# Performance work log

Measured on AMD Instinct MI355X. Metric: run time of the kernel, lower is better.

## Reference

```python
import jax, jax.numpy as jnp
import numpy as np

D_IN = 1024
D_OUT = 1024
NUM_HEAD = 16
HEAD_DIM = D_OUT // NUM_HEAD
CTX = 2048


def setup_inputs() -> dict:
    key = jax.random.key(0)
    ks = jax.random.split(key, 7)
    s = 0.02
    x = jax.random.normal(ks[0], (2, CTX, D_IN), dtype=jnp.float32)
    Wq = jax.random.normal(ks[1], (D_IN, D_OUT), dtype=jnp.float32) * s
    Wk = jax.random.normal(ks[2], (D_IN, D_OUT), dtype=jnp.float32) * s
    Wv = jax.random.normal(ks[3], (D_IN, D_OUT), dtype=jnp.float32) * s
    Wo = jax.random.normal(ks[4], (D_OUT, D_OUT), dtype=jnp.float32) * s
    bo = jax.random.normal(ks[5], (D_OUT,), dtype=jnp.float32) * s
    return {"x": x, "Wq": Wq, "Wk": Wk, "Wv": Wv, "Wo": Wo, "bo": bo}


def reference(x, Wq, Wk, Wv, Wo, bo):
    B, T, _ = x.shape
    # QKV projections, split into heads: [B, H, T, hd]
    def split_heads(y):
        return y.reshape(B, T, NUM_HEAD, HEAD_DIM).transpose(0, 2, 1, 3)
    q = split_heads(x @ Wq)
    k = split_heads(x @ Wk)
    v = split_heads(x @ Wv)
    # scaled causal attention scores [B, H, T, T]
    scores = jnp.einsum("bhqd,bhkd->bhqk", q, k) / jnp.sqrt(
        jnp.asarray(HEAD_DIM, dtype=x.dtype))
    causal = jnp.tril(jnp.ones((T, T), dtype=bool))  # mask buffer triu(diag=1) -> keep lower tri
    scores = jnp.where(causal[None, None], scores, jnp.asarray(-jnp.inf, dtype=x.dtype))
    attn = jax.nn.softmax(scores, axis=-1)
    # dropout with droprate=0.0 is identity
    ctx = jnp.einsum("bhqk,bhkd->bhqd", attn, v)
    ctx = ctx.transpose(0, 2, 1, 3).reshape(B, T, D_OUT)
    return ctx @ Wo + bo
```

## Files before the change

kernel.cpp:

```cpp
#include <hip/hip_runtime.h>

typedef __bf16 bf16x8 __attribute__((ext_vector_type(8)));
typedef float f32x4 __attribute__((ext_vector_type(4)));

__device__ inline unsigned short f2bf(float f) {
    unsigned int x = __builtin_bit_cast(unsigned int, f);
    x += 0x7fff + ((x >> 16) & 1);
    return (unsigned short)(x >> 16);
}

__device__ __forceinline__ void gl_lds16(const unsigned short* g, unsigned short* l)
{
    __builtin_amdgcn_global_load_lds(
        (const __attribute__((address_space(1))) void*)g,
        (__attribute__((address_space(3))) void*)l, 16, 0, 0);
}

__global__ __launch_bounds__(256)
void prep(const float* __restrict__ x, unsigned short* __restrict__ xb,
          const float* __restrict__ Wq, const float* __restrict__ Wk,
          const float* __restrict__ Wv, unsigned short* __restrict__ wT)
{
    __shared__ unsigned short T[64][72];
    if (blockIdx.x < 2048) {
        const size_t i = ((size_t)blockIdx.x * 256 + threadIdx.x) * 8;
        float4 a = *reinterpret_cast<const float4*>(x + i);
        float4 b = *reinterpret_cast<const float4*>(x + i + 4);
        unsigned short t[8] = { f2bf(a.x), f2bf(a.y), f2bf(a.z), f2bf(a.w),
                                f2bf(b.x), f2bf(b.y), f2bf(b.z), f2bf(b.w) };
        *reinterpret_cast<uint4*>(xb + i) = *reinterpret_cast<uint4*>(t);
        return;
    }
    const int blk = blockIdx.x - 2048;
    const int z = blk >> 8, within = blk & 255;
    const float* W = (z == 0) ? Wq : (z == 1) ? Wk : Wv;
    unsigned short* dstBase = wT + (size_t)z * 1024 * 1024;
    const int k0 = (within >> 4) * 64, n0 = (within & 15) * 64;
    const int r = threadIdx.x >> 2, c0 = (threadIdx.x & 3) * 16;
    const float* src = W + (size_t)(k0 + r) * 1024 + n0 + c0;
    #pragma unroll
    for (int j = 0; j < 16; j += 4) {
        float4 f = *reinterpret_cast<const float4*>(src + j);
        T[r][c0 + j]     = f2bf(f.x);
        T[r][c0 + j + 1] = f2bf(f.y);
        T[r][c0 + j + 2] = f2bf(f.z);
        T[r][c0 + j + 3] = f2bf(f.w);
    }
    __syncthreads();
    unsigned short* dst = dstBase + (size_t)(n0 + r) * 1024 + k0 + c0;
    #pragma unroll
    for (int h = 0; h < 2; ++h) {
        unsigned short t8[8];
        #pragma unroll
        for (int j = 0; j < 8; ++j) t8[j] = T[c0 + h * 8 + j][r];
        *reinterpret_cast<uint4*>(dst + h * 8) = *reinterpret_cast<uint4*>(t8);
    }
}

__global__ __launch_bounds__(256)
void wconv(const float* __restrict__ W, unsigned short* __restrict__ wT)
{
    __shared__ unsigned short T[64][72];
    const int k0 = blockIdx.y * 64, n0 = blockIdx.x * 64;
    const int r = threadIdx.x >> 2, c0 = (threadIdx.x & 3) * 16;
    const float* src = W + (size_t)(k0 + r) * 1024 + n0 + c0;
    #pragma unroll
    for (int j = 0; j < 16; j += 4) {
        float4 f = *reinterpret_cast<const float4*>(src + j);
        T[r][c0 + j]     = f2bf(f.x);
        T[r][c0 + j + 1] = f2bf(f.y);
        T[r][c0 + j + 2] = f2bf(f.z);
        T[r][c0 + j + 3] = f2bf(f.w);
    }
    __syncthreads();
    unsigned short* dst = wT + (size_t)(n0 + r) * 1024 + k0 + c0;
    #pragma unroll
    for (int h = 0; h < 2; ++h) {
        unsigned short t8[8];
        #pragma unroll
        for (int j = 0; j < 8; ++j) t8[j] = T[c0 + h * 8 + j][r];
        *reinterpret_cast<uint4*>(dst + h * 8) = *reinterpret_cast<uint4*>(t8);
    }
}

__global__ __launch_bounds__(256)
void gemm_qkv(const unsigned short* __restrict__ A,
              const unsigned short* __restrict__ BT,
              unsigned short* __restrict__ qb, unsigned short* __restrict__ kb,
              unsigned short* __restrict__ vT)
{
    __shared__ unsigned short As[128 * 32];
    __shared__ unsigned short Bs[128 * 32];

    const int tid = threadIdx.x;
    const int wave = tid >> 6, lane = tid & 63, quad = lane >> 4, l16 = lane & 15;
    const int wm = wave >> 1, wn = wave & 1;
    const int mBase = blockIdx.y * 128, nBase = blockIdx.x * 128;

    f32x4 acc[4][4] = {};

    const int srow = lane >> 2, sko = (lane & 3) * 8;

    for (int kb_ = 0; kb_ < 1024; kb_ += 32) {
        __syncthreads();
        #pragma unroll
        for (int j = 0; j < 2; ++j) {
            const int seg = wave * 2 + j;
            gl_lds16(A  + (size_t)(mBase + seg * 16 + srow) * 1024 + kb_ + sko,
                     As + seg * 512);
            gl_lds16(BT + (size_t)(nBase + seg * 16 + srow) * 1024 + kb_ + sko,
                     Bs + seg * 512);
        }
        __syncthreads();

        bf16x8 af[4], bf[4];
        #pragma unroll
        for (int t = 0; t < 4; ++t) {
            af[t] = *reinterpret_cast<const bf16x8*>(&As[(wm * 64 + t * 16 + l16) * 32 + quad * 8]);
            bf[t] = *reinterpret_cast<const bf16x8*>(&Bs[(wn * 64 + t * 16 + l16) * 32 + quad * 8]);
        }
        #pragma unroll
        for (int ti = 0; ti < 4; ++ti)
            #pragma unroll
            for (int tj = 0; tj < 4; ++tj)
                acc[ti][tj] = __builtin_amdgcn_mfma_f32_16x16x32_bf16(
                    af[ti], bf[tj], acc[ti][tj], 0, 0, 0);
    }

    #pragma unroll
    for (int ti = 0; ti < 4; ++ti) {
        const int row0 = mBase + wm * 64 + ti * 16 + quad * 4;
        #pragma unroll
        for (int tj = 0; tj < 4; ++tj) {
            const int col = nBase + wn * 64 + tj * 16 + l16;
            if (col < 1024) {
                #pragma unroll
                for (int i = 0; i < 4; ++i)
                    qb[(size_t)(row0 + i) * 1024 + col] = f2bf(acc[ti][tj][i]);
            } else if (col < 2048) {
                #pragma unroll
                for (int i = 0; i < 4; ++i)
                    kb[(size_t)(row0 + i) * 1024 + col - 1024] = f2bf(acc[ti][tj][i]);
            } else {
                unsigned short t4[4] = { f2bf(acc[ti][tj][0]), f2bf(acc[ti][tj][1]),
                                         f2bf(acc[ti][tj][2]), f2bf(acc[ti][tj][3]) };
                *reinterpret_cast<uint2*>(&vT[(size_t)(col - 2048) * 4096 + row0]) =
                    *reinterpret_cast<uint2*>(t4);
            }
        }
    }
}

__global__ __launch_bounds__(256)
void gemm_out64(const unsigned short* __restrict__ A,
                const unsigned short* __restrict__ BT,
                float* __restrict__ out, const float* __restrict__ bias)
{
    __shared__ unsigned short As[64 * 32];
    __shared__ unsigned short Bs[128 * 32];

    const int tid = threadIdx.x;
    const int wave = tid >> 6, lane = tid & 63, quad = lane >> 4, l16 = lane & 15;
    const int wm = wave >> 1, wn = wave & 1;
    const int mBase = blockIdx.y * 64, nBase = blockIdx.x * 128;

    f32x4 acc[2][4] = {};

    const int sa = lane >> 2, sb = (lane & 3) * 8;

    for (int kb = 0; kb < 1024; kb += 32) {
        __syncthreads();
        #pragma unroll
        for (int j = 0; j < 3; ++j) {
            const int op = wave * 3 + j;
            if (op < 4) {
                gl_lds16(A + (size_t)(mBase + op * 16 + sa) * 1024 + kb + sb,
                         As + op * 512);
            } else {
                const int rg = op - 4;
                gl_lds16(BT + (size_t)(nBase + rg * 16 + sa) * 1024 + kb + sb,
                         Bs + rg * 512);
            }
        }
        __syncthreads();

        bf16x8 af[2], bf[4];
        #pragma unroll
        for (int t = 0; t < 2; ++t)
            af[t] = *reinterpret_cast<const bf16x8*>(&As[(wm * 32 + t * 16 + l16) * 32 + quad * 8]);
        #pragma unroll
        for (int t = 0; t < 4; ++t)
            bf[t] = *reinterpret_cast<const bf16x8*>(&Bs[(wn * 64 + t * 16 + l16) * 32 + quad * 8]);
        #pragma unroll
        for (int ti = 0; ti < 2; ++ti)
            #pragma unroll
            for (int tj = 0; tj < 4; ++tj)
                acc[ti][tj] = __builtin_amdgcn_mfma_f32_16x16x32_bf16(
                    af[ti], bf[tj], acc[ti][tj], 0, 0, 0);
    }

    #pragma unroll
    for (int ti = 0; ti < 2; ++ti) {
        const int row0 = mBase + wm * 32 + ti * 16 + quad * 4;
        #pragma unroll
        for (int tj = 0; tj < 4; ++tj) {
            const int col = nBase + wn * 64 + tj * 16 + l16;
            const float ba = bias[col];
            #pragma unroll
            for (int i = 0; i < 4; ++i)
                out[(size_t)(row0 + i) * 1024 + col] = acc[ti][tj][i] + ba;
        }
    }
}

#define LDP 72

__global__ __launch_bounds__(256)
void attn6(const unsigned short* __restrict__ q,
           const unsigned short* __restrict__ k,
           const unsigned short* __restrict__ vT,
           unsigned short* __restrict__ ctx)
{
    __shared__ unsigned short Ks[2][2][64 * 32];
    __shared__ unsigned short Vs[2][2][64 * 32];
    __shared__ unsigned short PsA[64 * LDP];
    __shared__ unsigned short PsB[64 * LDP];

    const int tid  = threadIdx.x;
    const int wave = tid >> 6, lane = tid & 63, quad = lane >> 4, l16 = lane & 15;
    const int j  = blockIdx.x;
    const int bh = blockIdx.y;
    const int b = bh >> 4, h = bh & 15;
    const int tokBase = b * 2048;
    const int colBase = h * 64;
    const int qtA = 31 - j, qtB = j;
    const int qBaseA = qtA * 64, qBaseB = qtB * 64;

    bf16x8 aqA[2], aqB[2];
    {
        const unsigned short* qrA =
            q + (size_t)(tokBase + qBaseA + wave * 16 + l16) * 1024 + colBase;
        aqA[0] = *reinterpret_cast<const bf16x8*>(qrA + quad * 8);
        aqA[1] = *reinterpret_cast<const bf16x8*>(qrA + 32 + quad * 8);
        const unsigned short* qrB =
            q + (size_t)(tokBase + qBaseB + wave * 16 + l16) * 1024 + colBase;
        aqB[0] = *reinterpret_cast<const bf16x8*>(qrB + quad * 8);
        aqB[1] = *reinterpret_cast<const bf16x8*>(qrB + 32 + quad * 8);
    }

    f32x4 oA[4] = {}, oB[4] = {};
    float lsA[4] = {}, lsB[4] = {};

    const int sa = lane >> 2;
    const int sb = (lane & 3) * 8;

    auto stage = [&](int tok0, int buf) {
        #pragma unroll
        for (int o = 0; o < 2; ++o) {
            const int op = wave * 2 + o;
            const int hh = op >> 2, rg = op & 3;
            gl_lds16(k + (size_t)(tok0 + rg * 16 + sa) * 1024 + colBase + hh * 32 + sb,
                     &Ks[buf][hh][rg * 16 * 32]);
            gl_lds16(vT + (size_t)(colBase + rg * 16 + sa) * 4096 + tok0 + hh * 32 + sb,
                     &Vs[buf][hh][rg * 16 * 32]);
        }
    };

    stage(tokBase, 0);
    __syncthreads();

    const int nkt = qtA + 1;
    for (int kt = 0; kt < nkt; ++kt) {
        const int buf = kt & 1;
        if (kt + 1 < nkt)
            stage(tokBase + (kt + 1) * 64, buf ^ 1);

        const bool doB = (kt <= qtB);
        const bool diagA = (kt == qtA), diagB = (kt == qtB);

        {
            f32x4 sc[4] = {};
            #pragma unroll
            for (int t = 0; t < 4; ++t)
                #pragma unroll
                for (int kf = 0; kf < 2; ++kf) {
                    bf16x8 bk = *reinterpret_cast<const bf16x8*>(
                        &Ks[buf][kf][(t * 16 + l16) * 32 + quad * 8]);
                    sc[t] = __builtin_amdgcn_mfma_f32_16x16x32_bf16(aqA[kf], bk, sc[t], 0, 0, 0);
                }
            #pragma unroll
            for (int t = 0; t < 4; ++t) {
                const int ki = kt * 64 + t * 16 + l16;
                #pragma unroll
                for (int r = 0; r < 4; ++r) {
                    float p = __expf(sc[t][r] * 0.125f);
                    if (diagA && ki > qBaseA + wave * 16 + quad * 4 + r) p = 0.0f;
                    lsA[r] += p;
                    PsA[(wave * 16 + quad * 4 + r) * LDP + t * 16 + l16] = f2bf(p);
                }
            }
        }
        if (doB) {
            f32x4 sc[4] = {};
            #pragma unroll
            for (int t = 0; t < 4; ++t)
                #pragma unroll
                for (int kf = 0; kf < 2; ++kf) {
                    bf16x8 bk = *reinterpret_cast<const bf16x8*>(
                        &Ks[buf][kf][(t * 16 + l16) * 32 + quad * 8]);
                    sc[t] = __builtin_amdgcn_mfma_f32_16x16x32_bf16(aqB[kf], bk, sc[t], 0, 0, 0);
                }
            #pragma unroll
            for (int t = 0; t < 4; ++t) {
                const int ki = kt * 64 + t * 16 + l16;
                #pragma unroll
                for (int r = 0; r < 4; ++r) {
                    float p = __expf(sc[t][r] * 0.125f);
                    if (diagB && ki > qBaseB + wave * 16 + quad * 4 + r) p = 0.0f;
                    lsB[r] += p;
                    PsB[(wave * 16 + quad * 4 + r) * LDP + t * 16 + l16] = f2bf(p);
                }
            }
        }

        #pragma unroll
        for (int kf = 0; kf < 2; ++kf) {
            if (diagA && (wave * 16 + 15) < kf * 32) continue;
            bf16x8 ap = *reinterpret_cast<const bf16x8*>(
                &PsA[(wave * 16 + l16) * LDP + kf * 32 + quad * 8]);
            #pragma unroll
            for (int t = 0; t < 4; ++t) {
                bf16x8 bv = *reinterpret_cast<const bf16x8*>(
                    &Vs[buf][kf][(t * 16 + l16) * 32 + quad * 8]);
                oA[t] = __builtin_amdgcn_mfma_f32_16x16x32_bf16(ap, bv, oA[t], 0, 0, 0);
            }
        }
        if (doB) {
            #pragma unroll
            for (int kf = 0; kf < 2; ++kf) {
                if (diagB && (wave * 16 + 15) < kf * 32) continue;
                bf16x8 ap = *reinterpret_cast<const bf16x8*>(
                    &PsB[(wave * 16 + l16) * LDP + kf * 32 + quad * 8]);
                #pragma unroll
                for (int t = 0; t < 4; ++t) {
                    bf16x8 bv = *reinterpret_cast<const bf16x8*>(
                        &Vs[buf][kf][(t * 16 + l16) * 32 + quad * 8]);
                    oB[t] = __builtin_amdgcn_mfma_f32_16x16x32_bf16(ap, bv, oB[t], 0, 0, 0);
                }
            }
        }

        if (kt + 1 < nkt)
            __syncthreads();
    }

    #pragma unroll
    for (int off = 1; off < 16; off <<= 1)
        #pragma unroll
        for (int r = 0; r < 4; ++r) {
            lsA[r] += __shfl_xor(lsA[r], off);
            lsB[r] += __shfl_xor(lsB[r], off);
        }

    #pragma unroll
    for (int r = 0; r < 4; ++r) {
        const float invA = 1.0f / lsA[r];
        const float invB = 1.0f / lsB[r];
        const size_t grA = (size_t)(tokBase + qBaseA + wave * 16 + quad * 4 + r) * 1024 + colBase;
        const size_t grB = (size_t)(tokBase + qBaseB + wave * 16 + quad * 4 + r) * 1024 + colBase;
        #pragma unroll
        for (int t = 0; t < 4; ++t) {
            ctx[grA + t * 16 + l16] = f2bf(oA[t][r] * invA);
            ctx[grB + t * 16 + l16] = f2bf(oB[t][r] * invB);
        }
    }
}

extern "C" void kernel_launch(void* const* d_in, const int* in_sizes, int n_in,
                              void* d_out, int out_size, void* d_ws, size_t ws_size,
                              hipStream_t stream)
{
    const float* x  = (const float*)d_in[0];
    const float* Wq = (const float*)d_in[1];
    const float* Wk = (const float*)d_in[2];
    const float* Wv = (const float*)d_in[3];
    const float* Wo = (const float*)d_in[4];
    const float* bo = (const float*)d_in[5];
    float* out = (float*)d_out;

    unsigned short* xb     = (unsigned short*)d_ws;
    unsigned short* qb     = xb + (size_t)4096 * 1024;
    unsigned short* kb     = qb + (size_t)4096 * 1024;
    unsigned short* vT     = kb + (size_t)4096 * 1024;
    unsigned short* ctx    = xb;
    unsigned short* wqkvT  = (unsigned short*)d_out;
    unsigned short* woT    = kb;

    prep<<<2816, 256, 0, stream>>>(x, xb, Wq, Wk, Wv, wqkvT);

    gemm_qkv<<<dim3(24, 32), 256, 0, stream>>>(xb, wqkvT, qb, kb, vT);

    attn6<<<dim3(16, 32), 256, 0, stream>>>(qb, kb, vT, ctx);

    wconv<<<dim3(16, 16), 256, 0, stream>>>(Wo, woT);

    gemm_out64<<<dim3(8, 64), 256, 0, stream>>>(ctx, woT, out, bo);
}
```

Baseline: 194.7 us.

## Fuse Wo conversion into QKV GEMM launch and transpose V-tile MFMA for coalesced stores

Removes the separate wconv launch by appending 256 extra blocks to the QKV GEMM grid that convert and transpose Wo into bf16. The converted Wo is written into the Wq input buffer, since Wq has already been consumed by prep. The change also swaps the MFMA operand order for V tiles so each lane holds a column of V^T, giving row-contiguous stores into vT. This trades one launch and some serialization for overwriting an input buffer, which is only safe if inputs are not reused across calls, and for extra shared memory in the GEMM blocks.

```diff
diff --git a/kernel.cpp b/kernel.cpp
--- a/kernel.cpp
+++ b/kernel.cpp
@@ -58,44 +58,48 @@
 }
 
 __global__ __launch_bounds__(256)
-void wconv(const float* __restrict__ W, unsigned short* __restrict__ wT)
-{
-    __shared__ unsigned short T[64][72];
-    const int k0 = blockIdx.y * 64, n0 = blockIdx.x * 64;
-    const int r = threadIdx.x >> 2, c0 = (threadIdx.x & 3) * 16;
-    const float* src = W + (size_t)(k0 + r) * 1024 + n0 + c0;
-    #pragma unroll
-    for (int j = 0; j < 16; j += 4) {
-        float4 f = *reinterpret_cast<const float4*>(src + j);
-        T[r][c0 + j]     = f2bf(f.x);
-        T[r][c0 + j + 1] = f2bf(f.y);
-        T[r][c0 + j + 2] = f2bf(f.z);
-        T[r][c0 + j + 3] = f2bf(f.w);
-    }
-    __syncthreads();
-    unsigned short* dst = wT + (size_t)(n0 + r) * 1024 + k0 + c0;
-    #pragma unroll
-    for (int h = 0; h < 2; ++h) {
-        unsigned short t8[8];
-        #pragma unroll
-        for (int j = 0; j < 8; ++j) t8[j] = T[c0 + h * 8 + j][r];
-        *reinterpret_cast<uint4*>(dst + h * 8) = *reinterpret_cast<uint4*>(t8);
-    }
-}
-
-__global__ __launch_bounds__(256)
 void gemm_qkv(const unsigned short* __restrict__ A,
               const unsigned short* __restrict__ BT,
               unsigned short* __restrict__ qb, unsigned short* __restrict__ kb,
-              unsigned short* __restrict__ vT)
+              unsigned short* __restrict__ vT,
+              const float* __restrict__ Wo, unsigned short* __restrict__ woT)
 {
     __shared__ unsigned short As[128 * 32];
     __shared__ unsigned short Bs[128 * 32];
+    __shared__ unsigned short T[64][72];
 
     const int tid = threadIdx.x;
+
+    if (blockIdx.x >= 768) {
+        const int t = blockIdx.x - 768;
+        const int k0 = (t >> 4) * 64, n0 = (t & 15) * 64;
+        const int r = tid >> 2, c0 = (tid & 3) * 16;
+        const float* src = Wo + (size_t)(k0 + r) * 1024 + n0 + c0;
+        #pragma unroll
+        for (int j = 0; j < 16; j += 4) {
+            float4 f = *reinterpret_cast<const float4*>(src + j);
+            T[r][c0 + j]     = f2bf(f.x);
+            T[r][c0 + j + 1] = f2bf(f.y);
+            T[r][c0 + j + 2] = f2bf(f.z);
+            T[r][c0 + j + 3] = f2bf(f.w);
+        }
+        __syncthreads();
+        unsigned short* dst = woT + (size_t)(n0 + r) * 1024 + k0 + c0;
+        #pragma unroll
+        for (int h = 0; h < 2; ++h) {
+            unsigned short t8[8];
+            #pragma unroll
+            for (int j = 0; j < 8; ++j) t8[j] = T[c0 + h * 8 + j][r];
+            *reinterpret_cast<uint4*>(dst + h * 8) = *reinterpret_cast<uint4*>(t8);
+        }
+        return;
+    }
+
     const int wave = tid >> 6, lane = tid & 63, quad = lane >> 4, l16 = lane & 15;
     const int wm = wave >> 1, wn = wave & 1;
-    const int mBase = blockIdx.y * 128, nBase = blockIdx.x * 128;
+    const int nb = blockIdx.x % 24, mb = blockIdx.x / 24;
+    const int mBase = mb * 128, nBase = nb * 128;
+    const bool vsel = (nBase >= 2048);
 
     f32x4 acc[4][4] = {};
 
@@ -119,33 +123,51 @@
             af[t] = *reinterpret_cast<const bf16x8*>(&As[(wm * 64 + t * 16 + l16) * 32 + quad * 8]);
             bf[t] = *reinterpret_cast<const bf16x8*>(&Bs[(wn * 64 + t * 16 + l16) * 32 + quad * 8]);
         }
-        #pragma unroll
-        for (int ti = 0; ti < 4; ++ti)
-            #pragma unroll
-            for (int tj = 0; tj < 4; ++tj)
-                acc[ti][tj] = __builtin_amdgcn_mfma_f32_16x16x32_bf16(
-                    af[ti], bf[tj], acc[ti][tj], 0, 0, 0);
-    }
-
-    #pragma unroll
-    for (int ti = 0; ti < 4; ++ti) {
-        const int row0 = mBase + wm * 64 + ti * 16 + quad * 4;
-        #pragma unroll
-        for (int tj = 0; tj < 4; ++tj) {
-            const int col = nBase + wn * 64 + tj * 16 + l16;
-            if (col < 1024) {
+        if (!vsel) {
+            #pragma unroll
+            for (int ti = 0; ti < 4; ++ti)
+                #pragma unroll
+                for (int tj = 0; tj < 4; ++tj)
+                    acc[ti][tj] = __builtin_amdgcn_mfma_f32_16x16x32_bf16(
+                        af[ti], bf[tj], acc[ti][tj], 0, 0, 0);
+        } else {
+            #pragma unroll
+            for (int ti = 0; ti < 4; ++ti)
+                #pragma unroll
+                for (int tj = 0; tj < 4; ++tj)
+                    acc[ti][tj] = __builtin_amdgcn_mfma_f32_16x16x32_bf16(
+                        bf[tj], af[ti], acc[ti][tj], 0, 0, 0);
+        }
+    }
+
+    if (!vsel) {
+        #pragma unroll
+        for (int ti = 0; ti < 4; ++ti) {
+            const int row0 = mBase + wm * 64 + ti * 16 + quad * 4;
+            #pragma unroll
+            for (int tj = 0; tj < 4; ++tj) {
+                const int col = nBase + wn * 64 + tj * 16 + l16;
+                if (col < 1024) {
+                    #pragma unroll
+                    for (int i = 0; i < 4; ++i)
+                        qb[(size_t)(row0 + i) * 1024 + col] = f2bf(acc[ti][tj][i]);
+                } else {
+                    #pragma unroll
+                    for (int i = 0; i < 4; ++i)
+                        kb[(size_t)(row0 + i) * 1024 + col - 1024] = f2bf(acc[ti][tj][i]);
+                }
+            }
+        }
+    } else {
+        #pragma unroll
+        for (int ti = 0; ti < 4; ++ti) {
+            const int mcol = mBase + wm * 64 + ti * 16 + l16;
+            #pragma unroll
+            for (int tj = 0; tj < 4; ++tj) {
+                const int vrow0 = nBase - 2048 + wn * 64 + tj * 16 + quad * 4;
                 #pragma unroll
                 for (int i = 0; i < 4; ++i)
-                    qb[(size_t)(row0 + i) * 1024 + col] = f2bf(acc[ti][tj][i]);
-            } else if (col < 2048) {
-                #pragma unroll
-                for (int i = 0; i < 4; ++i)
-                    kb[(size_t)(row0 + i) * 1024 + col - 1024] = f2bf(acc[ti][tj][i]);
-            } else {
-                unsigned short t4[4] = { f2bf(acc[ti][tj][0]), f2bf(acc[ti][tj][1]),
-                                         f2bf(acc[ti][tj][2]), f2bf(acc[ti][tj][3]) };
-                *reinterpret_cast<uint2*>(&vT[(size_t)(col - 2048) * 4096 + row0]) =
-                    *reinterpret_cast<uint2*>(t4);
+                    vT[(size_t)(vrow0 + i) * 4096 + mcol] = f2bf(acc[ti][tj][i]);
             }
         }
     }
@@ -394,15 +416,13 @@
     unsigned short* vT     = kb + (size_t)4096 * 1024;
     unsigned short* ctx    = xb;
     unsigned short* wqkvT  = (unsigned short*)d_out;
-    unsigned short* woT    = kb;
+    unsigned short* woT    = (unsigned short*)d_in[1];
 
     prep<<<2816, 256, 0, stream>>>(x, xb, Wq, Wk, Wv, wqkvT);
 
-    gemm_qkv<<<dim3(24, 32), 256, 0, stream>>>(xb, wqkvT, qb, kb, vT);
+    gemm_qkv<<<1024, 256, 0, stream>>>(xb, wqkvT, qb, kb, vT, Wo, woT);
 
     attn6<<<dim3(16, 32), 256, 0, stream>>>(qb, kb, vT, ctx);
 
-    wconv<<<dim3(16, 16), 256, 0, stream>>>(Wo, woT);
-
     gemm_out64<<<dim3(8, 64), 256, 0, stream>>>(ctx, woT, out, bo);
 }
```

Result: slower. 203.1 us (+4.3%).
